# Kernel tuning notes

Hardware: AMD Instinct MI355X
Metric: run time of the kernel (lower is better)

## Reference

```python
import jax, jax.numpy as jnp
import numpy as np

N = 50000        # nodes
E = 1_600_000    # edges
D_IN = 256
H = 512          # hidden_dim (uniform)
N_CONVS = 2      # n_layers - 2
D_CAT = D_IN + H        # 768, GIN MLP input
D_MID = 2 * H           # 1024
D_SUM = H * 3           # sum(hidden_dim) = 1536
D_OUT = 256
LN_EPS = 1e-5


def _leaky(x):
    return jnp.where(x > 0, x, 0.1 * x)


def _layernorm(x, g, b):
    mu = jnp.mean(x, axis=-1, keepdims=True)
    var = jnp.var(x, axis=-1, keepdims=True)
    return (x - mu) * jax.lax.rsqrt(var + LN_EPS) * g + b


def setup_inputs() -> dict:
    key = jax.random.key(0)
    ks = jax.random.split(key, 16)

    def w(k, shape):
        fan_in = shape[-2] if len(shape) >= 2 else shape[-1]
        return jax.random.normal(k, shape, jnp.float32) / np.sqrt(fan_in)

    return {
        "x": jax.random.normal(ks[0], (N, D_IN), jnp.float32),
        "edge_index": jax.random.randint(ks[1], (2, E), 0, N, jnp.int32),
        "in_w": w(ks[2], (D_IN, H)),
        "in_b": jnp.zeros((H,), jnp.float32),
        # stacked per-conv params, leading dim = N_CONVS (identical shapes)
        "w1": w(ks[3], (N_CONVS, D_CAT, D_MID)),
        "b1": jnp.zeros((N_CONVS, D_MID), jnp.float32),
        "ln_g": jnp.ones((N_CONVS, D_MID), jnp.float32),
        "ln_b": jnp.zeros((N_CONVS, D_MID), jnp.float32),
        "w2": w(ks[4], (N_CONVS, D_MID, D_MID)),
        "b2": jnp.zeros((N_CONVS, D_MID), jnp.float32),
        "w3": w(ks[5], (N_CONVS, D_MID, H)),
        "b3": jnp.zeros((N_CONVS, H), jnp.float32),
        "out_w": w(ks[6], (D_SUM, D_OUT)),
        "out_b": jnp.zeros((D_OUT,), jnp.float32),
    }


def _gin_layer(x_cat, src, dst, w1, b1, g, bt, w2, b2, w3, b3):
    # GINConv with eps=0: mlp(x + sum_{j in N(i)} x_j); messages flow src -> dst
    agg = jax.ops.segment_sum(x_cat[src], dst, num_segments=N)
    h = x_cat + agg                       # [N, D_CAT]
    h = _leaky(_layernorm(h @ w1 + b1, g, bt))
    h = _leaky(h @ w2 + b2)
    return h @ w3 + b3                    # [N, H]


def reference(x, edge_index, in_w, in_b, w1, b1, ln_g, ln_b, w2, b2, w3, b3, out_w, out_b):
    src, dst = edge_index[0], edge_index[1]
    initial_x = x
    h = x @ in_w + in_b                   # in_proj: [N, H]
    hidden_states = [h]
    for i in range(N_CONVS):
        x_cat = jnp.concatenate([initial_x, h], axis=1)   # [N, D_CAT]
        h = _gin_layer(x_cat, src, dst, w1[i], b1[i], ln_g[i], ln_b[i],
                       w2[i], b2[i], w3[i], b3[i])
        hidden_states.append(h)
    hcat = jnp.concatenate(hidden_states, axis=1)         # [N, D_SUM]
    return hcat @ out_w + out_b                           # [N, D_OUT]
```

## Files before the change

kernel.cpp:

```cpp
#include <hip/hip_runtime.h>
#include <hip/hip_bf16.h>

#define NN 50000
#define DIN 256
#define HD 512
#define DCAT 768
#define DMID 1024
#define DSUM 1536
#define DOUT 256
#define CH 19200
#define LN_EPS 1e-5f

typedef __attribute__((ext_vector_type(8))) short short8;
typedef __attribute__((ext_vector_type(4))) float f32x4;
typedef __attribute__((ext_vector_type(2))) float f32x2;

__device__ __forceinline__ unsigned short f2b(float f) {
  unsigned int u = __float_as_uint(f);
  u += 0x7FFF + ((u >> 16) & 1);
  return (unsigned short)(u >> 16);
}
__device__ __forceinline__ float b2f(unsigned short s) {
  return __uint_as_float(((unsigned int)s) << 16);
}
__device__ __forceinline__ void splitbf(float v, unsigned short& hi, unsigned short& lo) {
  hi = f2b(v);
  lo = f2b(v - b2f(hi));
}
__device__ __forceinline__ unsigned char f2e4m3(float v) {
  return (unsigned char)(__builtin_amdgcn_cvt_pk_fp8_f32(v, v, 0, false) & 0xff);
}

__global__ void sentinel_fill(float* __restrict__ out, long n, float v) {
  for (long i = (long)blockIdx.x * blockDim.x + threadIdx.x; i < n;
       i += (long)gridDim.x * blockDim.x)
    out[i] = v;
}

__global__ void cast_split8_kernel(const float* __restrict__ in,
                                   unsigned short* __restrict__ oh,
                                   unsigned short* __restrict__ ol,
                                   unsigned char* __restrict__ o8, long n4) {
  for (long i = (long)blockIdx.x * blockDim.x + threadIdx.x; i < n4;
       i += (long)gridDim.x * blockDim.x) {
    float4 v = ((const float4*)in)[i];
    ushort4 h, l;
    splitbf(v.x, h.x, l.x); splitbf(v.y, h.y, l.y);
    splitbf(v.z, h.z, l.z); splitbf(v.w, h.w, l.w);
    ((ushort4*)oh)[i] = h;
    ((ushort4*)ol)[i] = l;
    unsigned int r = __builtin_amdgcn_cvt_pk_fp8_f32(v.x, v.y, 0, false);
    r = __builtin_amdgcn_cvt_pk_fp8_f32(v.z, v.w, r, true);
    ((unsigned int*)o8)[i] = r;
  }
}

template <bool SPLIT>
__global__ void cast_transpose_kernel(const float* __restrict__ in,
                                      unsigned short* __restrict__ oh,
                                      unsigned short* __restrict__ ol, int K, int N) {
  const float* src = in + (long)blockIdx.z * K * N;
  unsigned short* dh = oh + (long)blockIdx.z * K * N;
  unsigned short* dl = SPLIT ? ol + (long)blockIdx.z * K * N : nullptr;
  __shared__ unsigned short th[32][33];
  __shared__ unsigned short tl[SPLIT ? 32 : 1][33];
  int bk = blockIdx.x * 32, bn = blockIdx.y * 32;
  int tx = threadIdx.x & 31, ty = threadIdx.x >> 5;
#pragma unroll
  for (int i = ty; i < 32; i += 8) {
    float v = src[(long)(bk + i) * N + bn + tx];
    if (SPLIT) {
      unsigned short h, l;
      splitbf(v, h, l);
      th[i][tx] = h; tl[i][tx] = l;
    } else {
      th[i][tx] = f2b(v);
    }
  }
  __syncthreads();
#pragma unroll
  for (int i = ty; i < 32; i += 8) {
    dh[(long)(bn + i) * K + bk + tx] = th[tx][i];
    if (SPLIT) dl[(long)(bn + i) * K + bk + tx] = tl[tx][i];
  }
}

__global__ void deg_kernel(const int* __restrict__ dst, int E, int* __restrict__ rowptr) {
  int i = blockIdx.x * blockDim.x + threadIdx.x;
  if (i < E) atomicAdd(&rowptr[dst[i] + 1], 1);
}

__global__ void scan_block(int* __restrict__ data, int n, int* __restrict__ sums) {
  __shared__ int tmp[2][256];
  int i = blockIdx.x * 256 + threadIdx.x;
  int v = (i < n) ? data[i] : 0;
  int pp = 0;
  tmp[0][threadIdx.x] = v;
  __syncthreads();
#pragma unroll
  for (int off = 1; off < 256; off <<= 1) {
    int t2 = tmp[pp][threadIdx.x];
    if (threadIdx.x >= off) t2 += tmp[pp][threadIdx.x - off];
    tmp[pp ^ 1][threadIdx.x] = t2;
    pp ^= 1;
    __syncthreads();
  }
  if (i < n) data[i] = tmp[pp][threadIdx.x];
  if (threadIdx.x == 255) sums[blockIdx.x] = tmp[pp][255];
}

__global__ void scan_add(int* __restrict__ data, int n, const int* __restrict__ sums) {
  int i = blockIdx.x * 256 + threadIdx.x;
  if (blockIdx.x > 0 && i < n) data[i] += sums[blockIdx.x - 1];
}

__global__ void fill_kernel(const int* __restrict__ src, const int* __restrict__ dst, int E,
                            const int* __restrict__ rowptr, int* __restrict__ cursor,
                            int* __restrict__ cols) {
  int i = blockIdx.x * blockDim.x + threadIdx.x;
  if (i < E) {
    int r = dst[i];
    int p = rowptr[r] + atomicAdd(&cursor[r], 1);
    cols[p] = src[i];
  }
}

__global__ void agg_x_kernel(const unsigned short* __restrict__ xb,
                             const unsigned char* __restrict__ x8,
                             const int* __restrict__ rowptr,
                             const int* __restrict__ cols,
                             unsigned short* __restrict__ xpart) {
  int node = blockIdx.x * 4 + (threadIdx.x >> 6);
  int lane = threadIdx.x & 63;
  ushort4 own = *((const ushort4*)(xb + (long)node * DIN) + lane);
  float s0 = b2f(own.x), s1 = b2f(own.y), s2 = b2f(own.z), s3 = b2f(own.w);
  int e0 = rowptr[node], e1 = rowptr[node + 1];
  int p = e0;
#define XACC(w)                                                   \
  {                                                               \
    f32x2 t0 = __builtin_amdgcn_cvt_pk_f32_fp8((w), false);       \
    f32x2 t1 = __builtin_amdgcn_cvt_pk_f32_fp8((w), true);        \
    s0 += t0.x; s1 += t0.y; s2 += t1.x; s3 += t1.y;               \
  }
  for (; p + 3 < e1; p += 4) {
    int j0 = cols[p], j1 = cols[p + 1], j2 = cols[p + 2], j3 = cols[p + 3];
    unsigned int a = *((const unsigned int*)(x8 + (long)j0 * DIN) + lane);
    unsigned int b = *((const unsigned int*)(x8 + (long)j1 * DIN) + lane);
    unsigned int c = *((const unsigned int*)(x8 + (long)j2 * DIN) + lane);
    unsigned int d = *((const unsigned int*)(x8 + (long)j3 * DIN) + lane);
    XACC(a); XACC(b); XACC(c); XACC(d);
  }
  for (; p < e1; p++) {
    unsigned int a = *((const unsigned int*)(x8 + (long)cols[p] * DIN) + lane);
    XACC(a);
  }
#undef XACC
  ushort4 o;
  o.x = f2b(s0); o.y = f2b(s1); o.z = f2b(s2); o.w = f2b(s3);
  *((ushort4*)(xpart + (long)node * DIN) + lane) = o;
}

__global__ void agg_h_kernel(const unsigned short* __restrict__ h,
                             const unsigned char* __restrict__ h8,
                             const int* __restrict__ rowptr, const int* __restrict__ cols,
                             unsigned short* __restrict__ hpart) {
  int node = blockIdx.x * 4 + (threadIdx.x >> 6);
  int lane = threadIdx.x & 63;
  short8 own = *((const short8*)(h + (long)node * HD) + lane);
  float s[8];
#pragma unroll
  for (int q = 0; q < 8; q++) s[q] = b2f((unsigned short)own[q]);
  int e0 = rowptr[node], e1 = rowptr[node + 1];
  int p = e0;
#define HACC(w)                                                   \
  {                                                               \
    f32x2 t0 = __builtin_amdgcn_cvt_pk_f32_fp8((w).x, false);     \
    f32x2 t1 = __builtin_amdgcn_cvt_pk_f32_fp8((w).x, true);      \
    f32x2 t2 = __builtin_amdgcn_cvt_pk_f32_fp8((w).y, false);     \
    f32x2 t3 = __builtin_amdgcn_cvt_pk_f32_fp8((w).y, true);      \
    s[0] += t0.x; s[1] += t0.y; s[2] += t1.x; s[3] += t1.y;       \
    s[4] += t2.x; s[5] += t2.y; s[6] += t3.x; s[7] += t3.y;       \
  }
  for (; p + 3 < e1; p += 4) {
    int j0 = cols[p], j1 = cols[p + 1], j2 = cols[p + 2], j3 = cols[p + 3];
    uint2 a = *((const uint2*)(h8 + (long)j0 * HD) + lane);
    uint2 b = *((const uint2*)(h8 + (long)j1 * HD) + lane);
    uint2 c = *((const uint2*)(h8 + (long)j2 * HD) + lane);
    uint2 d = *((const uint2*)(h8 + (long)j3 * HD) + lane);
    HACC(a); HACC(b); HACC(c); HACC(d);
  }
  for (; p < e1; p++) {
    uint2 a = *((const uint2*)(h8 + (long)cols[p] * HD) + lane);
    HACC(a);
  }
#undef HACC
  short8 o;
#pragma unroll
  for (int q = 0; q < 8; q++) o[q] = (short)f2b(s[q]);
  *((short8*)(hpart + (long)node * HD) + lane) = o;
}

__global__ void ln_leaky_kernel(unsigned short* __restrict__ arr,
                                const float* __restrict__ gamma,
                                const float* __restrict__ beta) {
  int row = blockIdx.x, t = threadIdx.x;
  unsigned short* p = arr + (long)row * DMID;
  ushort4 u = ((const ushort4*)p)[t];
  float v0 = b2f(u.x), v1 = b2f(u.y), v2 = b2f(u.z), v3 = b2f(u.w);
  float s = v0 + v1 + v2 + v3;
  float sq = v0 * v0 + v1 * v1 + v2 * v2 + v3 * v3;
#pragma unroll
  for (int off = 32; off >= 1; off >>= 1) {
    s += __shfl_down(s, off, 64);
    sq += __shfl_down(sq, off, 64);
  }
  __shared__ float red[8];
  int w = t >> 6, lane = t & 63;
  if (lane == 0) { red[w] = s; red[4 + w] = sq; }
  __syncthreads();
  s = red[0] + red[1] + red[2] + red[3];
  sq = red[4] + red[5] + red[6] + red[7];
  float mean = s * (1.f / DMID);
  float var = sq * (1.f / DMID) - mean * mean;
  float rstd = rsqrtf(var + LN_EPS);
  float4 gv = ((const float4*)gamma)[t];
  float4 bv = ((const float4*)beta)[t];
  float o0 = (v0 - mean) * rstd * gv.x + bv.x;
  float o1 = (v1 - mean) * rstd * gv.y + bv.y;
  float o2 = (v2 - mean) * rstd * gv.z + bv.z;
  float o3 = (v3 - mean) * rstd * gv.w + bv.w;
  o0 = o0 > 0.f ? o0 : 0.1f * o0;
  o1 = o1 > 0.f ? o1 : 0.1f * o1;
  o2 = o2 > 0.f ? o2 : 0.1f * o2;
  o3 = o3 > 0.f ? o3 : 0.1f * o3;
  ushort4 ou;
  ou.x = f2b(o0); ou.y = f2b(o1); ou.z = f2b(o2); ou.w = f2b(o3);
  ((ushort4*)p)[t] = ou;
}

#define GLD16(src, dst)                                                          \
  __builtin_amdgcn_global_load_lds(                                              \
      (const __attribute__((address_space(1))) void*)(src),                      \
      (__attribute__((address_space(3))) void*)(dst), 16, 0, 0)

template <bool ACT, bool W8, int BK>
__launch_bounds__(256, 3)
__global__ void gemm1p(const unsigned short* __restrict__ Ah,
                       const unsigned short* __restrict__ A2h,
                       int lda, int lda2, int ksplit,
                       const unsigned short* __restrict__ Bh,
                       int ldb, const float* __restrict__ bias,
                       unsigned short* __restrict__ Chi,
                       unsigned char* __restrict__ C8,
                       int ldc, int M, int K, int NT) {
  const int lin = blockIdx.x;
  const int xcd = lin & 7;
  const int seq = lin >> 3;
  const int bn = seq % NT;
  const int bm = xcd + 8 * (seq / NT);
  if (bm * 128 >= M) return;

  constexpr int CT_LD = 136;
  constexpr int STAGE_B = 2 * 128 * BK * 2;
  constexpr int CT_B = 128 * CT_LD * 2;
  constexpr int C8_B = W8 ? 128 * CT_LD : 0;
  constexpr int SMEM_B = (STAGE_B > CT_B + C8_B) ? STAGE_B : (CT_B + C8_B);
  __shared__ __align__(16) unsigned char smem[SMEM_B];
  unsigned short* Ash = (unsigned short*)smem;
  unsigned short* Bsh = Ash + 128 * BK;
  const int t = threadIdx.x;
  const int l = t & 63;
  const int w = t >> 6;
  const int wm = w >> 1, wn = w & 1;
  const int lrow = l & 15, lk = (l >> 4) * 8;

  f32x4 acc[4][4] = {};

  const int arow0 = bm * 128;
  const int brow0 = bn * 128;

  for (int k0 = 0; k0 < K; k0 += BK) {
    const bool first = k0 < ksplit;
    const unsigned short* Abase = first ? Ah : A2h;
    const int acol = first ? k0 : (k0 - ksplit);
    const int alda = first ? lda : lda2;
    __syncthreads();
#pragma unroll
    for (int it = 0; it < BK / 16; it++) {
      int c = t + it * 256;
      int row = c / (BK / 8);
      int sk = (c % (BK / 8)) * 8;
      int ar = arow0 + row;
      if (ar >= M) ar = M - 1;
      int ldst = row * BK + sk;
      GLD16(Abase + (long)ar * alda + acol + sk, Ash + ldst);
      GLD16(Bh + (long)(brow0 + row) * ldb + k0 + sk, Bsh + ldst);
    }
    __syncthreads();
#pragma unroll
    for (int kk = 0; kk < BK / 32; kk++) {
      short8 ah[4], bh4[4];
#pragma unroll
      for (int m = 0; m < 4; m++)
        ah[m] = *(const short8*)(Ash + (wm * 64 + m * 16 + lrow) * BK + kk * 32 + lk);
#pragma unroll
      for (int n = 0; n < 4; n++)
        bh4[n] = *(const short8*)(Bsh + (wn * 64 + n * 16 + lrow) * BK + kk * 32 + lk);
#pragma unroll
      for (int m = 0; m < 4; m++)
#pragma unroll
        for (int n = 0; n < 4; n++)
          acc[m][n] = __builtin_amdgcn_mfma_f32_16x16x32_bf16(ah[m], bh4[n], acc[m][n], 0, 0, 0);
    }
  }

  __syncthreads();
  unsigned short* Ct = (unsigned short*)smem;
  unsigned char* C8t = smem + CT_B;
  const int orl = wm * 64 + (l >> 4) * 4;
  const int ocl = wn * 64 + lrow;
#pragma unroll
  for (int n = 0; n < 4; n++) {
    float bv = bias[bn * 128 + ocl + n * 16];
#pragma unroll
    for (int m = 0; m < 4; m++) {
#pragma unroll
      for (int ri = 0; ri < 4; ri++) {
        float v = acc[m][n][ri] + bv;
        if constexpr (ACT) v = v > 0.f ? v : 0.1f * v;
        int rr = orl + m * 16 + ri, cc = ocl + n * 16;
        Ct[rr * CT_LD + cc] = f2b(v);
        if constexpr (W8) C8t[rr * CT_LD + cc] = f2e4m3(v);
      }
    }
  }
  __syncthreads();
  const long row0 = bm * 128;
  const long col0 = bn * 128;
#pragma unroll
  for (int p = 0; p < 8; p++) {
    int idx = t + p * 256;
    int r = idx >> 4, cb = (idx & 15) * 8;
    long gr = row0 + r;
    if (gr < M)
      *(short8*)(Chi + gr * ldc + col0 + cb) = *(const short8*)(Ct + r * CT_LD + cb);
  }
  if constexpr (W8) {
#pragma unroll
    for (int p = 0; p < 8; p++) {
      int idx = t + p * 256;
      int r = idx >> 4, cb = (idx & 15) * 8;
      long gr = row0 + r;
      if (gr < M)
        *(uint2*)(C8 + gr * ldc + col0 + cb) = *(const uint2*)(C8t + r * CT_LD + cb);
    }
  }
}

template <int WMODE, bool AL, bool BL, bool ACC, bool W8, int OCC, int BK>
__launch_bounds__(256, OCC)
__global__ void gemmx(const unsigned short* __restrict__ Ah,
                      const unsigned short* __restrict__ Al,
                      int lda,
                      const unsigned short* __restrict__ Bh,
                      const unsigned short* __restrict__ Bl,
                      int ldb, const float* __restrict__ bias,
                      float* __restrict__ Cf,
                      unsigned short* __restrict__ Chi,
                      unsigned char* __restrict__ C8,
                      int ldc, int M, int K) {
  __shared__ __align__(16) unsigned short Ash[128 * BK];
  __shared__ __align__(16) unsigned short Asl[AL ? 128 * BK : 16];
  __shared__ __align__(16) unsigned short Bsh[128 * BK];
  __shared__ __align__(16) unsigned short Bsl[BL ? 128 * BK : 16];
  const int t = threadIdx.x;
  const int bm = blockIdx.x, bn = blockIdx.y;
  const int l = t & 63;
  const int w = t >> 6;
  const int wm = w >> 1, wn = w & 1;
  const int lrow = l & 15, lk = (l >> 4) * 8;

  f32x4 acc[4][4] = {};

  const int arow0 = bm * 128;
  const int brow0 = bn * 128;

  for (int k0 = 0; k0 < K; k0 += BK) {
    __syncthreads();
#pragma unroll
    for (int it = 0; it < BK / 16; it++) {
      int c = t + it * 256;
      int row = c / (BK / 8);
      int sk = (c % (BK / 8)) * 8;
      int ar = arow0 + row;
      if (ar >= M) ar = M - 1;
      long boff = (long)(brow0 + row) * ldb + k0 + sk;
      int ldst = row * BK + sk;
      GLD16(Ah + (long)ar * lda + k0 + sk, Ash + ldst);
      if (AL) GLD16(Al + (long)ar * lda + k0 + sk, Asl + ldst);
      GLD16(Bh + boff, Bsh + ldst);
      if (BL) GLD16(Bl + boff, Bsl + ldst);
    }
    __syncthreads();
#pragma unroll
    for (int kk = 0; kk < BK / 32; kk++) {
      short8 ah[4], al4[4], bh[4], bl4[4];
#pragma unroll
      for (int m = 0; m < 4; m++) {
        int ro = (wm * 64 + m * 16 + lrow) * BK + kk * 32 + lk;
        ah[m] = *(const short8*)(Ash + ro);
        if (AL) al4[m] = *(const short8*)(Asl + ro);
      }
#pragma unroll
      for (int n = 0; n < 4; n++) {
        int ro = (wn * 64 + n * 16 + lrow) * BK + kk * 32 + lk;
        bh[n] = *(const short8*)(Bsh + ro);
        if (BL) bl4[n] = *(const short8*)(Bsl + ro);
      }
#pragma unroll
      for (int m = 0; m < 4; m++)
#pragma unroll
        for (int n = 0; n < 4; n++) {
          acc[m][n] = __builtin_amdgcn_mfma_f32_16x16x32_bf16(ah[m], bh[n], acc[m][n], 0, 0, 0);
          if (BL)
            acc[m][n] = __builtin_amdgcn_mfma_f32_16x16x32_bf16(ah[m], bl4[n], acc[m][n], 0, 0, 0);
          if (AL)
            acc[m][n] = __builtin_amdgcn_mfma_f32_16x16x32_bf16(al4[m], bh[n], acc[m][n], 0, 0, 0);
        }
    }
  }

  const int orow0 = bm * 128 + wm * 64 + (l >> 4) * 4;
  const int ocol0 = bn * 128 + wn * 64 + lrow;
#pragma unroll
  for (int n = 0; n < 4; n++) {
    int gc = ocol0 + n * 16;
    float bv;
    if constexpr (ACC) bv = 0.f; else bv = bias[gc];
#pragma unroll
    for (int m = 0; m < 4; m++) {
#pragma unroll
      for (int ri = 0; ri < 4; ri++) {
        int gr = orow0 + m * 16 + ri;
        if (gr < M) {
          float v = acc[m][n][ri] + bv;
          if constexpr (ACC) v += Cf[(long)gr * ldc + gc];
          if constexpr (WMODE == 0) {
            Cf[(long)gr * ldc + gc] = v;
          } else {
            Chi[(long)gr * ldc + gc] = f2b(v);
            if constexpr (W8) C8[(long)gr * ldc + gc] = f2e4m3(v);
          }
        }
      }
    }
  }
}

extern "C" void kernel_launch(void* const* d_in, const int* in_sizes, int n_in,
                              void* d_out, int out_size, void* d_ws, size_t ws_size,
                              hipStream_t stream) {
  const float* x = (const float*)d_in[0];
  const int* ei = (const int*)d_in[1];
  const int E = in_sizes[1] / 2;
  const int* src = ei;
  const int* dst = ei + E;
  const float* in_w = (const float*)d_in[2];
  const float* in_b = (const float*)d_in[3];
  const float* w1 = (const float*)d_in[4];
  const float* b1 = (const float*)d_in[5];
  const float* ln_g = (const float*)d_in[6];
  const float* ln_b = (const float*)d_in[7];
  const float* w2 = (const float*)d_in[8];
  const float* b2 = (const float*)d_in[9];
  const float* w3 = (const float*)d_in[10];
  const float* b3 = (const float*)d_in[11];
  const float* out_w = (const float*)d_in[12];
  const float* out_b = (const float*)d_in[13];
  float* out = (float*)d_out;

  char* ws = (char*)d_ws;
  size_t off = 0;
  auto alloc = [&](size_t bytes) -> void* {
    void* p = ws + off;
    off += (bytes + 255) & ~(size_t)255;
    return p;
  };
  int* rowptr = (int*)alloc((NN + 1) * 4);
  int* cursor = (int*)alloc((size_t)NN * 4);
  int* cols = (int*)alloc((size_t)E * 4);
  int* sums = (int*)alloc(1024);
  int* sums2 = (int*)alloc(256);
  unsigned short* in_wb_h = (unsigned short*)alloc((size_t)HD * DIN * 2);
  unsigned short* in_wb_l = (unsigned short*)alloc((size_t)HD * DIN * 2);
  unsigned short* w1b = (unsigned short*)alloc(2ul * DMID * DCAT * 2);
  unsigned short* w2b = (unsigned short*)alloc(2ul * DMID * DMID * 2);
  unsigned short* w3b = (unsigned short*)alloc(2ul * HD * DMID * 2);
  unsigned short* out_wb_h = (unsigned short*)alloc((size_t)DOUT * DSUM * 2);
  unsigned short* out_wb_l = (unsigned short*)alloc((size_t)DOUT * DSUM * 2);
  unsigned short* xpart = (unsigned short*)alloc((size_t)NN * DIN * 2);
  unsigned short* h = (unsigned short*)alloc((size_t)NN * HD * 2);
  unsigned char* h8 = (unsigned char*)alloc((size_t)NN * HD);
  unsigned short* hpart = (unsigned short*)alloc((size_t)NN * HD * 2);
  unsigned short* h1c = (unsigned short*)alloc((size_t)CH * DMID * 2);
  unsigned short* h2c = (unsigned short*)alloc((size_t)CH * DMID * 2);
  const size_t need = off;

  if (need > ws_size) {
    sentinel_fill<<<2048, 256, 0, stream>>>(out, (long)NN * DOUT, (float)ws_size);
    return;
  }

  unsigned short* xb_h = hpart;
  unsigned short* xb_l = hpart + (size_t)NN * DIN;
  unsigned char* x8 = (unsigned char*)h1c;

  hipMemsetAsync(rowptr, 0, (NN + 1) * 4, stream);
  hipMemsetAsync(cursor, 0, (size_t)NN * 4, stream);

  const int eb = (E + 255) / 256;
  const int nscan = NN + 1;
  const int nsb = (nscan + 255) / 256;

  deg_kernel<<<eb, 256, 0, stream>>>(dst, E, rowptr);
  scan_block<<<nsb, 256, 0, stream>>>(rowptr, nscan, sums);
  scan_block<<<1, 256, 0, stream>>>(sums, nsb, sums2);
  scan_add<<<nsb, 256, 0, stream>>>(rowptr, nscan, sums);
  fill_kernel<<<eb, 256, 0, stream>>>(src, dst, E, rowptr, cursor, cols);

  cast_split8_kernel<<<2048, 256, 0, stream>>>(x, xb_h, xb_l, x8, (long)NN * DIN / 4);
  cast_transpose_kernel<true><<<dim3(DIN / 32, HD / 32, 1), 256, 0, stream>>>(in_w, in_wb_h, in_wb_l, DIN, HD);
  cast_transpose_kernel<false><<<dim3(DCAT / 32, DMID / 32, 2), 256, 0, stream>>>(w1, w1b, nullptr, DCAT, DMID);
  cast_transpose_kernel<false><<<dim3(DMID / 32, DMID / 32, 2), 256, 0, stream>>>(w2, w2b, nullptr, DMID, DMID);
  cast_transpose_kernel<false><<<dim3(DMID / 32, HD / 32, 2), 256, 0, stream>>>(w3, w3b, nullptr, DMID, HD);
  cast_transpose_kernel<true><<<dim3(DSUM / 32, DOUT / 32, 1), 256, 0, stream>>>(out_w, out_wb_h, out_wb_l, DSUM, DOUT);

  const int MT = (NN + 127) / 128;
  const int AGB = NN / 4;

  gemmx<1, true, true, false, true, 2, 64><<<dim3(MT, HD / 128), 256, 0, stream>>>(
      xb_h, xb_l, DIN, in_wb_h, in_wb_l, DIN, in_b,
      nullptr, h, h8, HD, NN, DIN);

  agg_x_kernel<<<AGB, 256, 0, stream>>>(xb_h, x8, rowptr, cols, xpart);

  gemmx<0, false, true, false, false, 2, 64><<<dim3(MT, DOUT / 128), 256, 0, stream>>>(
      h, nullptr, HD, out_wb_h, out_wb_l, DSUM, out_b,
      out, nullptr, nullptr, DOUT, NN, HD);

  for (int i = 0; i < 2; i++) {
    agg_h_kernel<<<AGB, 256, 0, stream>>>(h, h8, rowptr, cols, hpart);

    for (int r0 = 0; r0 < NN; r0 += CH) {
      int Mc = NN - r0 < CH ? NN - r0 : CH;
      int MTc = (Mc + 127) / 128;
      int MT8 = ((MTc + 7) / 8) * 8;
      gemm1p<false, false, 64><<<MT8 * (DMID / 128), 256, 0, stream>>>(
          xpart + (size_t)r0 * DIN, hpart + (size_t)r0 * HD, DIN, HD, DIN,
          w1b + (size_t)i * DMID * DCAT, DCAT,
          b1 + i * DMID, h1c, nullptr, DMID, Mc, DCAT, DMID / 128);
      ln_leaky_kernel<<<Mc, 256, 0, stream>>>(h1c, ln_g + i * DMID, ln_b + i * DMID);
      gemm1p<true, false, 64><<<MT8 * (DMID / 128), 256, 0, stream>>>(
          h1c, h1c, DMID, DMID, 1 << 30,
          w2b + (size_t)i * DMID * DMID, DMID,
          b2 + i * DMID, h2c, nullptr, DMID, Mc, DMID, DMID / 128);
      gemm1p<false, true, 64><<<MT8 * (HD / 128), 256, 0, stream>>>(
          h2c, h2c, DMID, DMID, 1 << 30,
          w3b + (size_t)i * HD * DMID, DMID,
          b3 + i * HD, h + (size_t)r0 * HD, h8 + (size_t)r0 * HD, HD, Mc, DMID, HD / 128);
    }

    gemmx<0, false, true, true, false, 2, 64><<<dim3(MT, DOUT / 128), 256, 0, stream>>>(
        h, nullptr, HD,
        out_wb_h + (size_t)(i + 1) * HD, out_wb_l + (size_t)(i + 1) * HD, DSUM,
        nullptr, out, nullptr, nullptr, DOUT, NN, HD);
  }
}
```

Before: 1.717 ms.

## Double-buffer LDS in gemm1p, add XOR swizzle, shrink BK to 32

The main MLP GEMM kernel now double-buffers its LDS tiles, issuing the next k-tile's global-to-LDS loads before computing the current one, which drops one barrier per iteration. Both GEMM kernels apply an XOR swizzle to the LDS chunk index to avoid bank conflicts on the MFMA fragment reads. The GIN MLP GEMMs switch from BK=64 to BK=32 so the doubled buffers still fit the shared-memory budget. The costs are more k-iterations and barrier syncs, and reliance on the async loads landing before the end-of-iteration barrier.

```diff
diff --git a/kernel.cpp b/kernel.cpp
--- a/kernel.cpp
+++ b/kernel.cpp
@@ -243,6 +243,12 @@
       (const __attribute__((address_space(1))) void*)(src),                      \
       (__attribute__((address_space(3))) void*)(dst), 16, 0, 0)
 
+template <int BK>
+__device__ __forceinline__ int swz(int row, int ch) {
+  if constexpr (BK == 64) return ch ^ (row & 7);
+  else return ch ^ ((row >> 1) & 3);
+}
+
 template <bool ACT, bool W8, int BK>
 __launch_bounds__(256, 3)
 __global__ void gemm1p(const unsigned short* __restrict__ Ah,
@@ -261,57 +267,69 @@
   if (bm * 128 >= M) return;
 
   constexpr int CT_LD = 136;
-  constexpr int STAGE_B = 2 * 128 * BK * 2;
+  constexpr int TILE = 128 * BK;
+  constexpr int STAGE_B = 2 * 2 * TILE * 2;
   constexpr int CT_B = 128 * CT_LD * 2;
   constexpr int C8_B = W8 ? 128 * CT_LD : 0;
   constexpr int SMEM_B = (STAGE_B > CT_B + C8_B) ? STAGE_B : (CT_B + C8_B);
   __shared__ __align__(16) unsigned char smem[SMEM_B];
   unsigned short* Ash = (unsigned short*)smem;
-  unsigned short* Bsh = Ash + 128 * BK;
+  unsigned short* Bsh = Ash + 2 * TILE;
   const int t = threadIdx.x;
   const int l = t & 63;
   const int w = t >> 6;
   const int wm = w >> 1, wn = w & 1;
-  const int lrow = l & 15, lk = (l >> 4) * 8;
+  const int lrow = l & 15;
 
   f32x4 acc[4][4] = {};
 
   const int arow0 = bm * 128;
   const int brow0 = bn * 128;
-
-  for (int k0 = 0; k0 < K; k0 += BK) {
+  constexpr int CPR = BK / 8;
+
+  auto STAGE = [&](int buf, int k0) {
     const bool first = k0 < ksplit;
     const unsigned short* Abase = first ? Ah : A2h;
     const int acol = first ? k0 : (k0 - ksplit);
     const int alda = first ? lda : lda2;
-    __syncthreads();
 #pragma unroll
     for (int it = 0; it < BK / 16; it++) {
       int c = t + it * 256;
-      int row = c / (BK / 8);
-      int sk = (c % (BK / 8)) * 8;
+      int row = c / CPR;
+      int pc = c % CPR;
+      int lc = swz<BK>(row, pc);
       int ar = arow0 + row;
       if (ar >= M) ar = M - 1;
-      int ldst = row * BK + sk;
-      GLD16(Abase + (long)ar * alda + acol + sk, Ash + ldst);
-      GLD16(Bh + (long)(brow0 + row) * ldb + k0 + sk, Bsh + ldst);
-    }
-    __syncthreads();
+      int ldst = buf * TILE + c * 8;
+      GLD16(Abase + (long)ar * alda + acol + lc * 8, Ash + ldst);
+      GLD16(Bh + (long)(brow0 + row) * ldb + k0 + lc * 8, Bsh + ldst);
+    }
+  };
+
+  const int nt = K / BK;
+  STAGE(0, 0);
+  __syncthreads();
+  int cur = 0;
+  for (int tk = 0; tk < nt; tk++) {
+    if (tk + 1 < nt) STAGE(cur ^ 1, (tk + 1) * BK);
 #pragma unroll
     for (int kk = 0; kk < BK / 32; kk++) {
+      const int ph = swz<BK>(lrow, kk * 4 + (l >> 4));
       short8 ah[4], bh4[4];
 #pragma unroll
       for (int m = 0; m < 4; m++)
-        ah[m] = *(const short8*)(Ash + (wm * 64 + m * 16 + lrow) * BK + kk * 32 + lk);
+        ah[m] = *(const short8*)(Ash + cur * TILE + (wm * 64 + m * 16 + lrow) * BK + ph * 8);
 #pragma unroll
       for (int n = 0; n < 4; n++)
-        bh4[n] = *(const short8*)(Bsh + (wn * 64 + n * 16 + lrow) * BK + kk * 32 + lk);
+        bh4[n] = *(const short8*)(Bsh + cur * TILE + (wn * 64 + n * 16 + lrow) * BK + ph * 8);
 #pragma unroll
       for (int m = 0; m < 4; m++)
 #pragma unroll
         for (int n = 0; n < 4; n++)
           acc[m][n] = __builtin_amdgcn_mfma_f32_16x16x32_bf16(ah[m], bh4[n], acc[m][n], 0, 0, 0);
     }
+    __syncthreads();
+    cur ^= 1;
   }
 
   __syncthreads();
@@ -378,7 +396,8 @@
   const int l = t & 63;
   const int w = t >> 6;
   const int wm = w >> 1, wn = w & 1;
-  const int lrow = l & 15, lk = (l >> 4) * 8;
+  const int lrow = l & 15;
+  constexpr int CPR = BK / 8;
 
   f32x4 acc[4][4] = {};
 
@@ -390,30 +409,32 @@
 #pragma unroll
     for (int it = 0; it < BK / 16; it++) {
       int c = t + it * 256;
-      int row = c / (BK / 8);
-      int sk = (c % (BK / 8)) * 8;
+      int row = c / CPR;
+      int pc = c % CPR;
+      int lc = swz<BK>(row, pc);
       int ar = arow0 + row;
       if (ar >= M) ar = M - 1;
-      long boff = (long)(brow0 + row) * ldb + k0 + sk;
-      int ldst = row * BK + sk;
-      GLD16(Ah + (long)ar * lda + k0 + sk, Ash + ldst);
-      if (AL) GLD16(Al + (long)ar * lda + k0 + sk, Asl + ldst);
+      long boff = (long)(brow0 + row) * ldb + k0 + lc * 8;
+      int ldst = row * BK + pc * 8;
+      GLD16(Ah + (long)ar * lda + k0 + lc * 8, Ash + ldst);
+      if (AL) GLD16(Al + (long)ar * lda + k0 + lc * 8, Asl + ldst);
       GLD16(Bh + boff, Bsh + ldst);
       if (BL) GLD16(Bl + boff, Bsl + ldst);
     }
     __syncthreads();
 #pragma unroll
     for (int kk = 0; kk < BK / 32; kk++) {
+      const int ph = swz<BK>(lrow, kk * 4 + (l >> 4));
       short8 ah[4], al4[4], bh[4], bl4[4];
 #pragma unroll
       for (int m = 0; m < 4; m++) {
-        int ro = (wm * 64 + m * 16 + lrow) * BK + kk * 32 + lk;
+        int ro = (wm * 64 + m * 16 + lrow) * BK + ph * 8;
         ah[m] = *(const short8*)(Ash + ro);
         if (AL) al4[m] = *(const short8*)(Asl + ro);
       }
 #pragma unroll
       for (int n = 0; n < 4; n++) {
-        int ro = (wn * 64 + n * 16 + lrow) * BK + kk * 32 + lk;
+        int ro = (wn * 64 + n * 16 + lrow) * BK + ph * 8;
         bh[n] = *(const short8*)(Bsh + ro);
         if (BL) bl4[n] = *(const short8*)(Bsl + ro);
       }
@@ -555,16 +576,16 @@
       int Mc = NN - r0 < CH ? NN - r0 : CH;
       int MTc = (Mc + 127) / 128;
       int MT8 = ((MTc + 7) / 8) * 8;
-      gemm1p<false, false, 64><<<MT8 * (DMID / 128), 256, 0, stream>>>(
+      gemm1p<false, false, 32><<<MT8 * (DMID / 128), 256, 0, stream>>>(
           xpart + (size_t)r0 * DIN, hpart + (size_t)r0 * HD, DIN, HD, DIN,
           w1b + (size_t)i * DMID * DCAT, DCAT,
           b1 + i * DMID, h1c, nullptr, DMID, Mc, DCAT, DMID / 128);
       ln_leaky_kernel<<<Mc, 256, 0, stream>>>(h1c, ln_g + i * DMID, ln_b + i * DMID);
-      gemm1p<true, false, 64><<<MT8 * (DMID / 128), 256, 0, stream>>>(
+      gemm1p<true, false, 32><<<MT8 * (DMID / 128), 256, 0, stream>>>(
           h1c, h1c, DMID, DMID, 1 << 30,
           w2b + (size_t)i * DMID * DMID, DMID,
           b2 + i * DMID, h2c, nullptr, DMID, Mc, DMID, DMID / 128);
-      gemm1p<false, true, 64><<<MT8 * (HD / 128), 256, 0, stream>>>(
+      gemm1p<false, true, 32><<<MT8 * (HD / 128), 256, 0, stream>>>(
           h2c, h2c, DMID, DMID, 1 << 30,
           w3b + (size_t)i * HD * DMID, DMID,
           b3 + i * HD, h + (size_t)r0 * HD, h8 + (size_t)r0 * HD, HD, Mc, DMID, HD / 128);
```

New measurement: 1.687 ms. No clear change (-1.8%).
